# Kernel tuning notes

Hardware: AMD Instinct MI355X
Metric: run time of the kernel (lower is better)

The kernel has to match this reference:

```python
import jax, jax.numpy as jnp
import numpy as np

B, S, H, F, E, K = 8, 4096, 256, 512, 16, 2
EPS = 1e-5


def setup_inputs() -> dict:
    key = jax.random.key(0)
    ks = jax.random.split(key, 9)
    sc = 0.02
    return {
        "x": jax.random.normal(ks[0], (B, S, H), dtype=jnp.float32),
        "gate_w": jax.random.normal(ks[1], (H, E), dtype=jnp.float32) * sc,
        "gate_b": jnp.zeros((E,), dtype=jnp.float32),
        "w1": jax.random.normal(ks[2], (E, H, F), dtype=jnp.float32) * sc,
        "b1": jnp.zeros((E, F), dtype=jnp.float32),
        "w2": jax.random.normal(ks[3], (E, F, H), dtype=jnp.float32) * sc,
        "b2": jnp.zeros((E, H), dtype=jnp.float32),
        "gamma": jnp.ones((H,), dtype=jnp.float32),
        "beta": jnp.zeros((H,), dtype=jnp.float32),
    }


def reference(x, gate_w, gate_b, w1, b1, w2, b2, gamma, beta):
    # gating: top-k over expert logits, softmax over the k selected logits
    gate_logits = x @ gate_w + gate_b                      # [B,S,E]
    topk_vals, topk_idx = jax.lax.top_k(gate_logits, K)    # [B,S,K]
    topk_w = jax.nn.softmax(topk_vals, axis=-1)            # [B,S,K]

    # naive dense MoE: every expert runs over every token (matches source)
    h = jax.nn.relu(jnp.einsum('bsh,ehf->bsef', x, w1) + b1)   # [B,S,E,F]
    expert_out = jnp.einsum('bsef,efh->bseh', h, w2) + b2       # [B,S,E,H]

    # select top-k expert outputs and combine with gate weights
    sel = jnp.take_along_axis(expert_out, topk_idx[:, :, :, None], axis=2)  # [B,S,K,H]
    moe = jnp.sum(topk_w[..., None] * sel, axis=2)              # [B,S,H]

    # residual + LayerNorm
    y = x + moe
    mu = jnp.mean(y, axis=-1, keepdims=True)
    var = jnp.var(y, axis=-1, keepdims=True)
    return (y - mu) / jnp.sqrt(var + EPS) * gamma + beta
```

## Files before the change

### kernel.cpp

```cpp
#include <hip/hip_runtime.h>
#include <hip/hip_bf16.h>

typedef __bf16 bf16_t;
typedef __bf16 bf16x8 __attribute__((ext_vector_type(8)));
typedef __bf16 bf16x4 __attribute__((ext_vector_type(4)));
typedef float f32x4 __attribute__((ext_vector_type(4)));

#define NB 8
#define NS 4096
#define NH 256
#define NF 512
#define NE 16
#define NTOK (NB*NS)
#define TT 64
#define NCH 16
#define XS_STRIDE 264
#define HS_STRIDE 40

__global__ __launch_bounds__(256) void transpose_kernel(
    const float* __restrict__ w1, const float* __restrict__ w2,
    bf16_t* __restrict__ w1t, bf16_t* __restrict__ w2t)
{
    __shared__ float tile[32][33];
    int bid = blockIdx.x;
    const float* src; bf16_t* dst; int R, C; int isw1;
    if (bid < 2048) { src = w1; dst = w1t; R = NH; C = NF; isw1 = 1; }
    else            { bid -= 2048; src = w2; dst = w2t; R = NF; C = NH; isw1 = 0; }
    const int tilesPerE = 128;
    int e = bid / tilesPerE;
    int t = bid % tilesPerE;
    int tcols = C / 32;
    int tr = (t / tcols) * 32, tc = (t % tcols) * 32;
    src += (size_t)e * R * C;
    dst += (size_t)e * R * C;
    int tx = threadIdx.x & 31, ty0 = threadIdx.x >> 5;
    #pragma unroll
    for (int i = 0; i < 4; i++) {
        int ty = ty0 + i * 8;
        tile[ty][tx] = src[(size_t)(tr + ty) * C + tc + tx];
    }
    __syncthreads();
    #pragma unroll
    for (int i = 0; i < 4; i++) {
        int ty = ty0 + i * 8;
        int drow = tc + ty;
        int dcol = tr + tx;
        size_t idx;
        if (isw1) {
            int swz = (((dcol >> 3) ^ (drow & 7)) << 3) | (dcol & 7);
            idx = (size_t)drow * NH + swz;
        } else {
            idx = (size_t)drow * R + dcol;
        }
        dst[idx] = (bf16_t)tile[tx][ty];
    }
}

__global__ __launch_bounds__(256) void gate_kernel(
    const float* __restrict__ x, const float* __restrict__ gate_w,
    const float* __restrict__ gate_b,
    int* __restrict__ counts, int* __restrict__ bucket_enc,
    float* __restrict__ bucket_gw, bf16_t* __restrict__ xb)
{
    __shared__ float gws[NH][NE];
    __shared__ int lcnt[NE];
    __shared__ int gbase[NE];

    for (int i = threadIdx.x; i < NH * NE; i += 256)
        gws[i >> 4][i & 15] = gate_w[i];
    if (threadIdx.x < NE) lcnt[threadIdx.x] = 0;
    __syncthreads();

    int   pe[2][2];
    int   po[2][2];
    float pg[2][2];
    int   toks[2];

    #pragma unroll
    for (int t = 0; t < 2; t++) {
        int tok = blockIdx.x * 512 + t * 256 + threadIdx.x;
        toks[t] = tok;
        const float4* xr = (const float4*)(x + (size_t)tok * NH);
        bf16x4* xbr = (bf16x4*)(xb + (size_t)tok * NH);
        float acc[NE];
        #pragma unroll
        for (int e = 0; e < NE; e++) acc[e] = gate_b[e];
        for (int h4 = 0; h4 < NH / 4; h4++) {
            float4 xv = xr[h4];
            bf16x4 xo;
            xo[0] = (bf16_t)xv.x; xo[1] = (bf16_t)xv.y;
            xo[2] = (bf16_t)xv.z; xo[3] = (bf16_t)xv.w;
            xbr[h4] = xo;
            #pragma unroll
            for (int j = 0; j < 4; j++) {
                float xs = (j == 0) ? xv.x : (j == 1) ? xv.y : (j == 2) ? xv.z : xv.w;
                int h = h4 * 4 + j;
                #pragma unroll
                for (int e = 0; e < NE; e++) acc[e] += xs * gws[h][e];
            }
        }
        float v0 = -1e30f, v1 = -1e30f; int i0 = 0, i1 = 0;
        #pragma unroll
        for (int e = 0; e < NE; e++) {
            float a = acc[e];
            if (a > v0)      { v1 = v0; i1 = i0; v0 = a; i0 = e; }
            else if (a > v1) { v1 = a; i1 = e; }
        }
        float e1 = __expf(v1 - v0);
        float s  = 1.f + e1;
        pe[t][0] = i0; pe[t][1] = i1;
        pg[t][0] = 1.f / s; pg[t][1] = e1 / s;
        po[t][0] = atomicAdd(&lcnt[i0], 1);
        po[t][1] = atomicAdd(&lcnt[i1], 1);
    }
    __syncthreads();
    if (threadIdx.x < NE)
        gbase[threadIdx.x] = atomicAdd(&counts[threadIdx.x], lcnt[threadIdx.x]);
    __syncthreads();
    #pragma unroll
    for (int t = 0; t < 2; t++)
        #pragma unroll
        for (int k = 0; k < 2; k++) {
            int e = pe[t][k];
            int pos = gbase[e] + po[t][k];
            bucket_enc[e * NTOK + pos] = toks[t] | (k << 20);
            bucket_gw [e * NTOK + pos] = pg[t][k];
        }
}

__global__ __launch_bounds__(256, 2) void moe_kernel(
    const bf16_t* __restrict__ xb,
    const bf16_t* __restrict__ w1t,
    const float*  __restrict__ b1,
    const bf16_t* __restrict__ w2t,
    const float*  __restrict__ b2,
    const int* __restrict__ counts,
    const int* __restrict__ bucket_enc,
    const float* __restrict__ bucket_gw,
    bf16_t* __restrict__ pairbuf)
{
    __shared__ __align__(16) bf16_t Xs[TT][XS_STRIDE];
    __shared__ uint4 W1s4[2][1024];
    __shared__ __align__(16) bf16_t Hs[2][TT][HS_STRIDE];
    __shared__ int   tok_s[TT];
    __shared__ float gw_s[TT];

    int flat = blockIdx.x;
    int e     = (flat & 7) * 2 + ((flat >> 3) & 1);
    int tile0 = flat >> 4;
    int n_e = counts[e];
    int wave = threadIdx.x >> 6;
    int lane = threadIdx.x & 63;
    int l15 = lane & 15, q = lane >> 4;

    const bf16_t* w1te = w1t + (size_t)e * NF * NH;
    const bf16_t* w2te = w2t + (size_t)e * NH * NF;

    int ntiles = (n_e + TT - 1) / TT;
    for (int tile = tile0; tile < ntiles; tile += 64) {
        int tstart = tile * TT;
        __syncthreads();
        if (threadIdx.x < TT) {
            int slot = tstart + threadIdx.x;
            if (slot < n_e) {
                tok_s[threadIdx.x] = bucket_enc[e * NTOK + slot];
                gw_s [threadIdx.x] = bucket_gw [e * NTOK + slot];
            } else { tok_s[threadIdx.x] = 0; gw_s[threadIdx.x] = 0.f; }
        }
        __syncthreads();
        {
            int c  = threadIdx.x & 31;
            int r0 = threadIdx.x >> 5;
            #pragma unroll
            for (int i = 0; i < 8; i++) {
                int r = r0 + i * 8;
                int tok = tok_s[r] & 0xFFFFF;
                const uint4* src = (const uint4*)(xb + (size_t)tok * NH) + c;
                *(uint4*)&Xs[r][c * 8] = *src;
            }
            const uint4* gw1 = (const uint4*)w1te;
            #pragma unroll
            for (int i = 0; i < 4; i++)
                W1s4[0][i * 256 + threadIdx.x] = gw1[i * 256 + threadIdx.x];
        }
        __syncthreads();

        f32x4 oacc[4][4];
        #pragma unroll
        for (int a = 0; a < 4; a++)
            #pragma unroll
            for (int b = 0; b < 4; b++) { f32x4 z = {0.f,0.f,0.f,0.f}; oacc[a][b] = z; }

        for (int ch = 0; ch < NCH; ch++) {
            int buf = ch & 1;
            uint4 pf[4];
            bool do_pf = (ch + 1 < NCH);
            if (do_pf) {
                const uint4* gw1 = (const uint4*)(w1te + (size_t)(ch + 1) * 32 * NH);
                #pragma unroll
                for (int i = 0; i < 4; i++) pf[i] = gw1[i * 256 + threadIdx.x];
            }
            bf16x8 bf2[4];
            #pragma unroll
            for (int nt = 0; nt < 4; nt++) {
                int hh = wave * 64 + nt * 16 + l15;
                bf2[nt] = *(const bf16x8*)&w2te[(size_t)hh * NF + ch * 32 + q * 8];
            }
            f32x4 hacc[2]; { f32x4 z = {0.f,0.f,0.f,0.f}; hacc[0] = z; hacc[1] = z; }
            const bf16_t* w1s = (const bf16_t*)W1s4[buf];
            #pragma unroll
            for (int ks = 0; ks < NH / 32; ks++) {
                bf16x8 afrag = *(const bf16x8*)&Xs[wave * 16 + l15][ks * 32 + q * 8];
                #pragma unroll
                for (int n = 0; n < 2; n++) {
                    int fl = n * 16 + l15;
                    bf16x8 bfrag = *(const bf16x8*)&w1s[fl * NH + ((((ks * 4 + q) ^ (fl & 7))) << 3)];
                    hacc[n] = __builtin_amdgcn_mfma_f32_16x16x32_bf16(afrag, bfrag, hacc[n], 0, 0, 0);
                }
            }
            #pragma unroll
            for (int n = 0; n < 2; n++) {
                int f = ch * 32 + n * 16 + l15;
                float bv = b1[e * NF + f];
                #pragma unroll
                for (int r = 0; r < 4; r++) {
                    float v = hacc[n][r] + bv;
                    v = v > 0.f ? v : 0.f;
                    Hs[buf][wave * 16 + q * 4 + r][n * 16 + l15] = (bf16_t)v;
                }
            }
            if (do_pf) {
                #pragma unroll
                for (int i = 0; i < 4; i++)
                    W1s4[buf ^ 1][i * 256 + threadIdx.x] = pf[i];
            }
            __syncthreads();
            #pragma unroll
            for (int mt = 0; mt < 4; mt++) {
                bf16x8 afrag = *(const bf16x8*)&Hs[buf][mt * 16 + l15][q * 8];
                #pragma unroll
                for (int nt = 0; nt < 4; nt++) {
                    oacc[mt][nt] = __builtin_amdgcn_mfma_f32_16x16x32_bf16(afrag, bf2[nt], oacc[mt][nt], 0, 0, 0);
                }
            }
        }
        #pragma unroll
        for (int nt = 0; nt < 4; nt++) {
            int col = wave * 64 + nt * 16 + l15;
            float b2v = b2[e * NH + col];
            #pragma unroll
            for (int mt = 0; mt < 4; mt++) {
                #pragma unroll
                for (int r = 0; r < 4; r++) {
                    int row = mt * 16 + q * 4 + r;
                    if (tstart + row < n_e) {
                        int enc = tok_s[row];
                        int tok = enc & 0xFFFFF;
                        int k   = enc >> 20;
                        float v = (oacc[mt][nt][r] + b2v) * gw_s[row];
                        pairbuf[((size_t)(tok * 2 + k)) * NH + col] = (bf16_t)v;
                    }
                }
            }
        }
    }
}

__global__ __launch_bounds__(256) void ln_kernel(
    const float* __restrict__ x, const bf16_t* __restrict__ pairbuf,
    const float* __restrict__ gamma, const float* __restrict__ beta,
    float* __restrict__ out)
{
    int tok = blockIdx.x;
    int h = threadIdx.x;
    float y = x[(size_t)tok * NH + h]
            + (float)pairbuf[(size_t)(tok * 2) * NH + h]
            + (float)pairbuf[(size_t)(tok * 2 + 1) * NH + h];
    float s = y, s2 = y * y;
    #pragma unroll
    for (int o = 32; o > 0; o >>= 1) { s += __shfl_down(s, o); s2 += __shfl_down(s2, o); }
    __shared__ float red[8];
    int wave = threadIdx.x >> 6, lane = threadIdx.x & 63;
    if (lane == 0) { red[wave] = s; red[4 + wave] = s2; }
    __syncthreads();
    if (threadIdx.x == 0) {
        float ts  = red[0] + red[1] + red[2] + red[3];
        float ts2 = red[4] + red[5] + red[6] + red[7];
        float mu  = ts / NH;
        float var = ts2 / NH - mu * mu;
        red[0] = mu;
        red[1] = rsqrtf(var + 1e-5f);
    }
    __syncthreads();
    float mu = red[0], rstd = red[1];
    out[(size_t)tok * NH + h] = ((y - mu) * rstd) * gamma[h] + beta[h];
}

extern "C" void kernel_launch(void* const* d_in, const int* in_sizes, int n_in,
                              void* d_out, int out_size, void* d_ws, size_t ws_size,
                              hipStream_t stream) {
    const float* x      = (const float*)d_in[0];
    const float* gate_w = (const float*)d_in[1];
    const float* gate_b = (const float*)d_in[2];
    const float* w1     = (const float*)d_in[3];
    const float* b1     = (const float*)d_in[4];
    const float* w2     = (const float*)d_in[5];
    const float* b2     = (const float*)d_in[6];
    const float* gamma  = (const float*)d_in[7];
    const float* beta   = (const float*)d_in[8];
    float* out = (float*)d_out;

    char* ws = (char*)d_ws;
    const size_t MB = 1024 * 1024;
    int*    counts     = (int*)ws;
    int*    bucket_enc = (int*)(ws + 256);
    float*  bucket_gw  = (float*)(ws + 256 + 2 * MB);
    bf16_t* w1t        = (bf16_t*)(ws + 256 + 4 * MB);
    bf16_t* w2t        = (bf16_t*)(ws + 256 + 8 * MB);
    bf16_t* xb         = (bf16_t*)(ws + 256 + 12 * MB);
    bf16_t* pairbuf    = (bf16_t*)(ws + 256 + 28 * MB);

    hipMemsetAsync(counts, 0, 256, stream);
    transpose_kernel<<<4096, 256, 0, stream>>>(w1, w2, w1t, w2t);
    gate_kernel<<<64, 256, 0, stream>>>(x, gate_w, gate_b, counts, bucket_enc, bucket_gw, xb);
    moe_kernel<<<1024, 256, 0, stream>>>(xb, w1t, b1, w2t, b2, counts, bucket_enc, bucket_gw, pairbuf);
    ln_kernel<<<NTOK, 256, 0, stream>>>(x, pairbuf, gamma, beta, out);
}
```

Measured before the change: 278.9 us.

## Restructure MoE GEMM pipeline, deterministic bucketing, and wave-per-token LayerNorm

The expert kernel is restructured. It drops the LDS staging of gathered X rows and reads X fragments directly from global memory. W1 is staged in 64-wide F chunks via global_load_lds, with a new swizzled layout, a 2x2 wave tiling for GEMM1, and a W2 layout that gives coalesced fragment loads. Occupancy rises to 3 blocks per SM with a 768-block grid. Gating now uses per-block counts, a scan kernel and a separate scatter kernel in place of global atomics, which makes bucket order deterministic at the cost of two extra launches. LayerNorm processes one token per wave with float4 loads and shuffle-only reductions, removing the syncthreads.

```diff
diff --git a/kernel.cpp b/kernel.cpp
--- a/kernel.cpp
+++ b/kernel.cpp
@@ -13,9 +13,7 @@
 #define NE 16
 #define NTOK (NB*NS)
 #define TT 64
-#define NCH 16
-#define XS_STRIDE 264
-#define HS_STRIDE 40
+#define EW (NF*NH)
 
 __global__ __launch_bounds__(256) void transpose_kernel(
     const float* __restrict__ w1, const float* __restrict__ w2,
@@ -32,7 +30,7 @@
     int tcols = C / 32;
     int tr = (t / tcols) * 32, tc = (t % tcols) * 32;
     src += (size_t)e * R * C;
-    dst += (size_t)e * R * C;
+    dst += (size_t)e * EW;
     int tx = threadIdx.x & 31, ty0 = threadIdx.x >> 5;
     #pragma unroll
     for (int i = 0; i < 4; i++) {
@@ -47,10 +45,12 @@
         int dcol = tr + tx;
         size_t idx;
         if (isw1) {
-            int swz = (((dcol >> 3) ^ (drow & 7)) << 3) | (dcol & 7);
-            idx = (size_t)drow * NH + swz;
+            int c = drow >> 6, fl = drow & 63;
+            int g = dcol >> 3;
+            int gs = (g & 24) | ((g ^ fl) & 7);
+            idx = c * 16384 + fl * 256 + gs * 8 + (dcol & 7);
         } else {
-            idx = (size_t)drow * R + dcol;
+            idx = (size_t)(dcol >> 3) * 2048 + drow * 8 + (dcol & 7);
         }
         dst[idx] = (bf16_t)tile[tx][ty];
     }
@@ -59,76 +59,93 @@
 __global__ __launch_bounds__(256) void gate_kernel(
     const float* __restrict__ x, const float* __restrict__ gate_w,
     const float* __restrict__ gate_b,
-    int* __restrict__ counts, int* __restrict__ bucket_enc,
-    float* __restrict__ bucket_gw, bf16_t* __restrict__ xb)
-{
-    __shared__ float gws[NH][NE];
+    int* __restrict__ blockcnt,
+    int* __restrict__ pick_e, int* __restrict__ pick_r,
+    float2* __restrict__ pick_w, bf16_t* __restrict__ xb)
+{
+    __shared__ float gws[NH * NE];
     __shared__ int lcnt[NE];
-    __shared__ int gbase[NE];
-
-    for (int i = threadIdx.x; i < NH * NE; i += 256)
-        gws[i >> 4][i & 15] = gate_w[i];
+
+    for (int i = threadIdx.x; i < NH * NE; i += 256) gws[i] = gate_w[i];
     if (threadIdx.x < NE) lcnt[threadIdx.x] = 0;
     __syncthreads();
 
-    int   pe[2][2];
-    int   po[2][2];
-    float pg[2][2];
-    int   toks[2];
-
-    #pragma unroll
-    for (int t = 0; t < 2; t++) {
-        int tok = blockIdx.x * 512 + t * 256 + threadIdx.x;
-        toks[t] = tok;
-        const float4* xr = (const float4*)(x + (size_t)tok * NH);
-        bf16x4* xbr = (bf16x4*)(xb + (size_t)tok * NH);
-        float acc[NE];
+    int tok = blockIdx.x * 256 + threadIdx.x;
+    const float4* xr = (const float4*)(x + (size_t)tok * NH);
+    bf16x4* xbr = (bf16x4*)(xb + (size_t)tok * NH);
+    float acc[NE];
+    #pragma unroll
+    for (int e = 0; e < NE; e++) acc[e] = gate_b[e];
+    #pragma unroll 4
+    for (int h4 = 0; h4 < NH / 4; h4++) {
+        float4 xv = xr[h4];
+        bf16x4 xo;
+        xo[0] = (bf16_t)xv.x; xo[1] = (bf16_t)xv.y;
+        xo[2] = (bf16_t)xv.z; xo[3] = (bf16_t)xv.w;
+        xbr[h4] = xo;
         #pragma unroll
-        for (int e = 0; e < NE; e++) acc[e] = gate_b[e];
-        for (int h4 = 0; h4 < NH / 4; h4++) {
-            float4 xv = xr[h4];
-            bf16x4 xo;
-            xo[0] = (bf16_t)xv.x; xo[1] = (bf16_t)xv.y;
-            xo[2] = (bf16_t)xv.z; xo[3] = (bf16_t)xv.w;
-            xbr[h4] = xo;
+        for (int j = 0; j < 4; j++) {
+            float xs = (j == 0) ? xv.x : (j == 1) ? xv.y : (j == 2) ? xv.z : xv.w;
+            const float* g = &gws[(h4 * 4 + j) * NE];
             #pragma unroll
-            for (int j = 0; j < 4; j++) {
-                float xs = (j == 0) ? xv.x : (j == 1) ? xv.y : (j == 2) ? xv.z : xv.w;
-                int h = h4 * 4 + j;
-                #pragma unroll
-                for (int e = 0; e < NE; e++) acc[e] += xs * gws[h][e];
-            }
-        }
-        float v0 = -1e30f, v1 = -1e30f; int i0 = 0, i1 = 0;
-        #pragma unroll
-        for (int e = 0; e < NE; e++) {
-            float a = acc[e];
-            if (a > v0)      { v1 = v0; i1 = i0; v0 = a; i0 = e; }
-            else if (a > v1) { v1 = a; i1 = e; }
-        }
-        float e1 = __expf(v1 - v0);
-        float s  = 1.f + e1;
-        pe[t][0] = i0; pe[t][1] = i1;
-        pg[t][0] = 1.f / s; pg[t][1] = e1 / s;
-        po[t][0] = atomicAdd(&lcnt[i0], 1);
-        po[t][1] = atomicAdd(&lcnt[i1], 1);
-    }
+            for (int e = 0; e < NE; e++) acc[e] += xs * g[e];
+        }
+    }
+    float v0 = -1e30f, v1 = -1e30f; int i0 = 0, i1 = 0;
+    #pragma unroll
+    for (int e = 0; e < NE; e++) {
+        float a = acc[e];
+        if (a > v0)      { v1 = v0; i1 = i0; v0 = a; i0 = e; }
+        else if (a > v1) { v1 = a; i1 = e; }
+    }
+    float e1 = __expf(v1 - v0);
+    float s  = 1.f + e1;
+    int r0 = atomicAdd(&lcnt[i0], 1);
+    int r1 = atomicAdd(&lcnt[i1], 1);
+    pick_e[tok] = i0 | (i1 << 8);
+    pick_r[tok] = r0 | (r1 << 16);
+    pick_w[tok] = make_float2(1.f / s, e1 / s);
     __syncthreads();
     if (threadIdx.x < NE)
-        gbase[threadIdx.x] = atomicAdd(&counts[threadIdx.x], lcnt[threadIdx.x]);
+        blockcnt[threadIdx.x * 128 + blockIdx.x] = lcnt[threadIdx.x];
+}
+
+__global__ __launch_bounds__(256) void scan_kernel(
+    const int* __restrict__ blockcnt, int* __restrict__ segb,
+    int* __restrict__ counts)
+{
+    __shared__ int cnts[NE * 128];
+    for (int i = threadIdx.x; i < NE * 128; i += 256) cnts[i] = blockcnt[i];
     __syncthreads();
-    #pragma unroll
-    for (int t = 0; t < 2; t++)
-        #pragma unroll
-        for (int k = 0; k < 2; k++) {
-            int e = pe[t][k];
-            int pos = gbase[e] + po[t][k];
-            bucket_enc[e * NTOK + pos] = toks[t] | (k << 20);
-            bucket_gw [e * NTOK + pos] = pg[t][k];
-        }
-}
-
-__global__ __launch_bounds__(256, 2) void moe_kernel(
+    if (threadIdx.x < NE) {
+        int e = threadIdx.x, run = 0;
+        for (int b = 0; b < 128; b++) {
+            segb[e * 128 + b] = run;
+            run += cnts[e * 128 + b];
+        }
+        counts[e] = run;
+    }
+}
+
+__global__ __launch_bounds__(256) void scatter_kernel(
+    const int* __restrict__ pick_e, const int* __restrict__ pick_r,
+    const float2* __restrict__ pick_w, const int* __restrict__ segb,
+    int* __restrict__ bucket_enc, float* __restrict__ bucket_gw)
+{
+    int tok = blockIdx.x * 256 + threadIdx.x;
+    int blk = tok >> 8;
+    int pe = pick_e[tok], pr = pick_r[tok];
+    float2 w = pick_w[tok];
+    int e0 = pe & 255, e1 = (pe >> 8) & 255;
+    int p0 = segb[e0 * 128 + blk] + (pr & 0xFFFF);
+    int p1 = segb[e1 * 128 + blk] + (pr >> 16);
+    bucket_enc[e0 * NTOK + p0] = tok;
+    bucket_gw [e0 * NTOK + p0] = w.x;
+    bucket_enc[e1 * NTOK + p1] = tok | (1 << 20);
+    bucket_gw [e1 * NTOK + p1] = w.y;
+}
+
+__global__ __launch_bounds__(256, 3) void moe_kernel(
     const bf16_t* __restrict__ xb,
     const bf16_t* __restrict__ w1t,
     const float*  __restrict__ b1,
@@ -139,9 +156,8 @@
     const float* __restrict__ bucket_gw,
     bf16_t* __restrict__ pairbuf)
 {
-    __shared__ __align__(16) bf16_t Xs[TT][XS_STRIDE];
-    __shared__ uint4 W1s4[2][1024];
-    __shared__ __align__(16) bf16_t Hs[2][TT][HS_STRIDE];
+    __shared__ __align__(16) bf16_t W1s[64 * 256];
+    __shared__ __align__(16) bf16_t Hs[2][64 * 64];
     __shared__ int   tok_s[TT];
     __shared__ float gw_s[TT];
 
@@ -152,12 +168,14 @@
     int wave = threadIdx.x >> 6;
     int lane = threadIdx.x & 63;
     int l15 = lane & 15, q = lane >> 4;
-
-    const bf16_t* w1te = w1t + (size_t)e * NF * NH;
-    const bf16_t* w2te = w2t + (size_t)e * NH * NF;
+    int mbase = (wave & 1) * 32;
+    int nbase = (wave >> 1) * 32;
+
+    const bf16_t* w1te = w1t + (size_t)e * EW;
+    const bf16_t* w2te = w2t + (size_t)e * EW;
 
     int ntiles = (n_e + TT - 1) / TT;
-    for (int tile = tile0; tile < ntiles; tile += 64) {
+    for (int tile = tile0; tile < ntiles; tile += 48) {
         int tstart = tile * TT;
         __syncthreads();
         if (threadIdx.x < TT) {
@@ -168,22 +186,10 @@
             } else { tok_s[threadIdx.x] = 0; gw_s[threadIdx.x] = 0.f; }
         }
         __syncthreads();
-        {
-            int c  = threadIdx.x & 31;
-            int r0 = threadIdx.x >> 5;
-            #pragma unroll
-            for (int i = 0; i < 8; i++) {
-                int r = r0 + i * 8;
-                int tok = tok_s[r] & 0xFFFFF;
-                const uint4* src = (const uint4*)(xb + (size_t)tok * NH) + c;
-                *(uint4*)&Xs[r][c * 8] = *src;
-            }
-            const uint4* gw1 = (const uint4*)w1te;
-            #pragma unroll
-            for (int i = 0; i < 4; i++)
-                W1s4[0][i * 256 + threadIdx.x] = gw1[i * 256 + threadIdx.x];
-        }
-        __syncthreads();
+
+        const bf16_t* xr0 = xb + (size_t)(tok_s[mbase + l15] & 0xFFFFF) * NH + q * 8;
+        const bf16_t* xr1 = xb + (size_t)(tok_s[mbase + 16 + l15] & 0xFFFFF) * NH + q * 8;
+        int fl0 = nbase + l15, fl1 = nbase + 16 + l15;
 
         f32x4 oacc[4][4];
         #pragma unroll
@@ -191,59 +197,96 @@
             #pragma unroll
             for (int b = 0; b < 4; b++) { f32x4 z = {0.f,0.f,0.f,0.f}; oacc[a][b] = z; }
 
-        for (int ch = 0; ch < NCH; ch++) {
-            int buf = ch & 1;
-            uint4 pf[4];
-            bool do_pf = (ch + 1 < NCH);
-            if (do_pf) {
-                const uint4* gw1 = (const uint4*)(w1te + (size_t)(ch + 1) * 32 * NH);
-                #pragma unroll
-                for (int i = 0; i < 4; i++) pf[i] = gw1[i * 256 + threadIdx.x];
-            }
-            bf16x8 bf2[4];
-            #pragma unroll
-            for (int nt = 0; nt < 4; nt++) {
-                int hh = wave * 64 + nt * 16 + l15;
-                bf2[nt] = *(const bf16x8*)&w2te[(size_t)hh * NF + ch * 32 + q * 8];
-            }
-            f32x4 hacc[2]; { f32x4 z = {0.f,0.f,0.f,0.f}; hacc[0] = z; hacc[1] = z; }
-            const bf16_t* w1s = (const bf16_t*)W1s4[buf];
-            #pragma unroll
-            for (int ks = 0; ks < NH / 32; ks++) {
-                bf16x8 afrag = *(const bf16x8*)&Xs[wave * 16 + l15][ks * 32 + q * 8];
-                #pragma unroll
-                for (int n = 0; n < 2; n++) {
-                    int fl = n * 16 + l15;
-                    bf16x8 bfrag = *(const bf16x8*)&w1s[fl * NH + ((((ks * 4 + q) ^ (fl & 7))) << 3)];
-                    hacc[n] = __builtin_amdgcn_mfma_f32_16x16x32_bf16(afrag, bfrag, hacc[n], 0, 0, 0);
-                }
-            }
-            #pragma unroll
-            for (int n = 0; n < 2; n++) {
-                int f = ch * 32 + n * 16 + l15;
-                float bv = b1[e * NF + f];
-                #pragma unroll
-                for (int r = 0; r < 4; r++) {
-                    float v = hacc[n][r] + bv;
-                    v = v > 0.f ? v : 0.f;
-                    Hs[buf][wave * 16 + q * 4 + r][n * 16 + l15] = (bf16_t)v;
-                }
-            }
-            if (do_pf) {
-                #pragma unroll
-                for (int i = 0; i < 4; i++)
-                    W1s4[buf ^ 1][i * 256 + threadIdx.x] = pf[i];
-            }
+        #define STAGE_W1(CH) do {                                            \
+            const bf16_t* gch = w1te + (CH) * 16384;                         \
+            _Pragma("unroll")                                                \
+            for (int i = 0; i < 8; i++) {                                    \
+                int seg = wave * 8 + i;                                      \
+                __builtin_amdgcn_global_load_lds(                            \
+                    (const __attribute__((address_space(1))) void*)          \
+                        (gch + seg * 512 + lane * 8),                        \
+                    (__attribute__((address_space(3))) void*)(&W1s[seg * 512]), \
+                    16, 0, 0);                                               \
+            }                                                                \
+        } while (0)
+
+        #define GEMM1(CH) do {                                               \
+            f32x4 hacc[2][2];                                                \
+            _Pragma("unroll")                                                \
+            for (int a = 0; a < 2; a++)                                      \
+                _Pragma("unroll")                                            \
+                for (int b = 0; b < 2; b++) { f32x4 z = {0.f,0.f,0.f,0.f}; hacc[a][b] = z; } \
+            _Pragma("unroll 4")                                              \
+            for (int ks = 0; ks < 8; ks++) {                                 \
+                bf16x8 af0 = *(const bf16x8*)(xr0 + ks * 32);                \
+                bf16x8 af1 = *(const bf16x8*)(xr1 + ks * 32);                \
+                int g = ks * 4 + q;                                          \
+                bf16x8 bf0 = *(const bf16x8*)&W1s[fl0 * 256 + (((g & 24) | ((g ^ fl0) & 7)) << 3)]; \
+                bf16x8 bf1 = *(const bf16x8*)&W1s[fl1 * 256 + (((g & 24) | ((g ^ fl1) & 7)) << 3)]; \
+                hacc[0][0] = __builtin_amdgcn_mfma_f32_16x16x32_bf16(af0, bf0, hacc[0][0], 0, 0, 0); \
+                hacc[1][0] = __builtin_amdgcn_mfma_f32_16x16x32_bf16(af1, bf0, hacc[1][0], 0, 0, 0); \
+                hacc[0][1] = __builtin_amdgcn_mfma_f32_16x16x32_bf16(af0, bf1, hacc[0][1], 0, 0, 0); \
+                hacc[1][1] = __builtin_amdgcn_mfma_f32_16x16x32_bf16(af1, bf1, hacc[1][1], 0, 0, 0); \
+            }                                                                \
+            int buf = (CH) & 1;                                              \
+            float b1v0 = b1[e * NF + (CH) * 64 + fl0];                       \
+            float b1v1 = b1[e * NF + (CH) * 64 + fl1];                       \
+            _Pragma("unroll")                                                \
+            for (int ni = 0; ni < 2; ni++) {                                 \
+                int col = nbase + ni * 16 + l15;                             \
+                int cg = col >> 3;                                           \
+                float bv = ni ? b1v1 : b1v0;                                 \
+                _Pragma("unroll")                                            \
+                for (int mi = 0; mi < 2; mi++) {                             \
+                    _Pragma("unroll")                                        \
+                    for (int r = 0; r < 4; r++) {                            \
+                        int row = mbase + mi * 16 + q * 4 + r;               \
+                        float v = hacc[mi][ni][r] + bv;                      \
+                        v = v > 0.f ? v : 0.f;                               \
+                        Hs[buf][row * 64 + ((cg ^ (row & 7)) << 3) + (col & 7)] = (bf16_t)v; \
+                    }                                                        \
+                }                                                            \
+            }                                                                \
+        } while (0)
+
+        #define GEMM2(CH) do {                                               \
+            int buf = (CH) & 1;                                              \
+            _Pragma("unroll")                                                \
+            for (int ks2 = 0; ks2 < 2; ks2++) {                              \
+                bf16x8 af2[4], bf2[4];                                       \
+                _Pragma("unroll")                                            \
+                for (int mt = 0; mt < 4; mt++) {                             \
+                    int row = mt * 16 + l15;                                 \
+                    int cg = ks2 * 4 + q;                                    \
+                    af2[mt] = *(const bf16x8*)&Hs[buf][row * 64 + ((cg ^ (row & 7)) << 3)]; \
+                }                                                            \
+                _Pragma("unroll")                                            \
+                for (int nt = 0; nt < 4; nt++) {                             \
+                    int hh = wave * 64 + nt * 16 + l15;                      \
+                    bf2[nt] = *(const bf16x8*)&w2te[((size_t)((CH) * 8 + ks2 * 4 + q)) * 2048 + hh * 8]; \
+                }                                                            \
+                _Pragma("unroll")                                            \
+                for (int mt = 0; mt < 4; mt++)                               \
+                    _Pragma("unroll")                                        \
+                    for (int nt = 0; nt < 4; nt++)                           \
+                        oacc[mt][nt] = __builtin_amdgcn_mfma_f32_16x16x32_bf16(af2[mt], bf2[nt], oacc[mt][nt], 0, 0, 0); \
+            }                                                                \
+        } while (0)
+
+        STAGE_W1(0);
+        __syncthreads();
+        GEMM1(0);
+        __syncthreads();
+        #pragma unroll 1
+        for (int ch = 1; ch < 8; ch++) {
+            STAGE_W1(ch);
+            GEMM2(ch - 1);
             __syncthreads();
-            #pragma unroll
-            for (int mt = 0; mt < 4; mt++) {
-                bf16x8 afrag = *(const bf16x8*)&Hs[buf][mt * 16 + l15][q * 8];
-                #pragma unroll
-                for (int nt = 0; nt < 4; nt++) {
-                    oacc[mt][nt] = __builtin_amdgcn_mfma_f32_16x16x32_bf16(afrag, bf2[nt], oacc[mt][nt], 0, 0, 0);
-                }
-            }
-        }
+            GEMM1(ch);
+            __syncthreads();
+        }
+        GEMM2(7);
+
         #pragma unroll
         for (int nt = 0; nt < 4; nt++) {
             int col = wave * 64 + nt * 16 + l15;
@@ -263,6 +306,9 @@
                 }
             }
         }
+        #undef STAGE_W1
+        #undef GEMM1
+        #undef GEMM2
     }
 }
 
@@ -271,29 +317,34 @@
     const float* __restrict__ gamma, const float* __restrict__ beta,
     float* __restrict__ out)
 {
-    int tok = blockIdx.x;
-    int h = threadIdx.x;
-    float y = x[(size_t)tok * NH + h]
-            + (float)pairbuf[(size_t)(tok * 2) * NH + h]
-            + (float)pairbuf[(size_t)(tok * 2 + 1) * NH + h];
-    float s = y, s2 = y * y;
-    #pragma unroll
-    for (int o = 32; o > 0; o >>= 1) { s += __shfl_down(s, o); s2 += __shfl_down(s2, o); }
-    __shared__ float red[8];
     int wave = threadIdx.x >> 6, lane = threadIdx.x & 63;
-    if (lane == 0) { red[wave] = s; red[4 + wave] = s2; }
-    __syncthreads();
-    if (threadIdx.x == 0) {
-        float ts  = red[0] + red[1] + red[2] + red[3];
-        float ts2 = red[4] + red[5] + red[6] + red[7];
-        float mu  = ts / NH;
-        float var = ts2 / NH - mu * mu;
-        red[0] = mu;
-        red[1] = rsqrtf(var + 1e-5f);
-    }
-    __syncthreads();
-    float mu = red[0], rstd = red[1];
-    out[(size_t)tok * NH + h] = ((y - mu) * rstd) * gamma[h] + beta[h];
+    int tok = blockIdx.x * 4 + wave;
+    float4 xv = ((const float4*)(x + (size_t)tok * NH))[lane];
+    bf16x4 p0 = ((const bf16x4*)(pairbuf + (size_t)(tok * 2) * NH))[lane];
+    bf16x4 p1 = ((const bf16x4*)(pairbuf + (size_t)(tok * 2 + 1) * NH))[lane];
+    float4 y;
+    y.x = xv.x + (float)p0[0] + (float)p1[0];
+    y.y = xv.y + (float)p0[1] + (float)p1[1];
+    y.z = xv.z + (float)p0[2] + (float)p1[2];
+    y.w = xv.w + (float)p0[3] + (float)p1[3];
+    float s  = y.x + y.y + y.z + y.w;
+    float s2 = y.x*y.x + y.y*y.y + y.z*y.z + y.w*y.w;
+    #pragma unroll
+    for (int o = 32; o > 0; o >>= 1) {
+        s  += __shfl_xor(s, o);
+        s2 += __shfl_xor(s2, o);
+    }
+    float mu  = s * (1.f / NH);
+    float var = s2 * (1.f / NH) - mu * mu;
+    float rstd = rsqrtf(var + 1e-5f);
+    float4 g4 = ((const float4*)gamma)[lane];
+    float4 b4 = ((const float4*)beta)[lane];
+    float4 o4;
+    o4.x = (y.x - mu) * rstd * g4.x + b4.x;
+    o4.y = (y.y - mu) * rstd * g4.y + b4.y;
+    o4.z = (y.z - mu) * rstd * g4.z + b4.z;
+    o4.w = (y.w - mu) * rstd * g4.w + b4.w;
+    ((float4*)(out + (size_t)tok * NH))[lane] = o4;
 }
 
 extern "C" void kernel_launch(void* const* d_in, const int* in_sizes, int n_in,
@@ -311,18 +362,27 @@
     float* out = (float*)d_out;
 
     char* ws = (char*)d_ws;
-    const size_t MB = 1024 * 1024;
+    const size_t KB = 1024, MB = 1024 * 1024;
     int*    counts     = (int*)ws;
-    int*    bucket_enc = (int*)(ws + 256);
-    float*  bucket_gw  = (float*)(ws + 256 + 2 * MB);
-    bf16_t* w1t        = (bf16_t*)(ws + 256 + 4 * MB);
-    bf16_t* w2t        = (bf16_t*)(ws + 256 + 8 * MB);
-    bf16_t* xb         = (bf16_t*)(ws + 256 + 12 * MB);
-    bf16_t* pairbuf    = (bf16_t*)(ws + 256 + 28 * MB);
-
-    hipMemsetAsync(counts, 0, 256, stream);
+    int*    blockcnt   = (int*)(ws + 4  * KB);
+    int*    segb       = (int*)(ws + 12 * KB);
+    int*    pick_e     = (int*)(ws + 64 * KB);
+    int*    pick_r     = (int*)(ws + 192 * KB);
+    float2* pick_w     = (float2*)(ws + 320 * KB);
+    int*    bucket_enc = (int*)(ws + 1 * MB);
+    float*  bucket_gw  = (float*)(ws + 3 * MB);
+    bf16_t* w1t        = (bf16_t*)(ws + 5 * MB);
+    bf16_t* w2t        = (bf16_t*)(ws + 9 * MB);
+    bf16_t* xb         = (bf16_t*)(ws + 13 * MB);
+    bf16_t* pairbuf    = (bf16_t*)(ws + 29 * MB);
+
     transpose_kernel<<<4096, 256, 0, stream>>>(w1, w2, w1t, w2t);
-    gate_kernel<<<64, 256, 0, stream>>>(x, gate_w, gate_b, counts, bucket_enc, bucket_gw, xb);
-    moe_kernel<<<1024, 256, 0, stream>>>(xb, w1t, b1, w2t, b2, counts, bucket_enc, bucket_gw, pairbuf);
-    ln_kernel<<<NTOK, 256, 0, stream>>>(x, pairbuf, gamma, beta, out);
-}
+    gate_kernel<<<128, 256, 0, stream>>>(x, gate_w, gate_b, blockcnt,
+                                         pick_e, pick_r, pick_w, xb);
+    scan_kernel<<<1, 256, 0, stream>>>(blockcnt, segb, counts);
+    scatter_kernel<<<128, 256, 0, stream>>>(pick_e, pick_r, pick_w, segb,
+                                            bucket_enc, bucket_gw);
+    moe_kernel<<<768, 256, 0, stream>>>(xb, w1t, b1, w2t, b2, counts,
+                                        bucket_enc, bucket_gw, pairbuf);
+    ln_kernel<<<NTOK / 4, 256, 0, stream>>>(x, pairbuf, gamma, beta, out);
+}
```

Result: slower. 302.0 us (+8.3%).
